# Optimization experiments

Measured on AMD Instinct MI355X. Metric: run time of the kernel, lower is better.

The kernel has to match this reference:

```python
import jax, jax.numpy as jnp
import numpy as np

H = 4      # heads
D = 32     # per-head / input channel dim
B, N = 1, 256


def setup_inputs() -> dict:
    key = jax.random.key(0)
    ks = jax.random.split(key, 10)
    x = jax.random.normal(ks[0], (B, N, N, D), dtype=jnp.float32)
    # binary key mask (1 = keep, 0 = masked out)
    mask = (jax.random.uniform(ks[1], (B, N, N)) > 0.15).astype(jnp.float32)
    s = 1.0 / np.sqrt(D)
    Wq = jax.random.normal(ks[2], (H * D, D), dtype=jnp.float32) * s
    bq = jnp.zeros((H * D,), dtype=jnp.float32)
    Wk = jax.random.normal(ks[3], (H * D, D), dtype=jnp.float32) * s
    bk = jnp.zeros((H * D,), dtype=jnp.float32)
    Wv = jax.random.normal(ks[4], (H * D, D), dtype=jnp.float32) * s
    bv = jnp.zeros((H * D,), dtype=jnp.float32)
    Wb = jax.random.normal(ks[5], (H, D), dtype=jnp.float32) * s
    bb = jnp.zeros((H,), dtype=jnp.float32)
    return {"x": x, "mask": mask, "Wq": Wq, "bq": bq, "Wk": Wk, "bk": bk,
            "Wv": Wv, "bv": bv, "Wb": Wb, "bb": bb}


def reference(x, mask, Wq, bq, Wk, bk, Wv, bv, Wb, bb):
    b_, i_, j_, d_ = x.shape
    # QKV projections -> [B, I, J, H, D]
    q = (x @ Wq.T + bq).reshape(b_, i_, j_, H, d_)
    k = (x @ Wk.T + bk).reshape(b_, i_, j_, H, d_)
    v = (x @ Wv.T + bv).reshape(b_, i_, j_, H, d_)
    # pairwise triangle bias: [B, I, J, H] -> [B, H, J, K]
    tri_b = jnp.transpose(x @ Wb.T + bb, (0, 3, 1, 2))
    scale = 1.0 / jnp.sqrt(jnp.asarray(d_, x.dtype))
    # scores over the key index k along the row: [B, H, I, J, K]
    scores = jnp.einsum('bijhd,bikhd->bhijk', q, k) * scale
    scores = scores + tri_b[:, :, None, :, :]                 # triangle bias
    scores = scores + (mask - 1.0)[:, None, :, None, :] * 1e9  # key mask
    attn = jax.nn.softmax(scores, axis=-1)
    out = jnp.einsum('bhijk,bikhd->bijhd', attn, v)  # [B, I, J, H, D]
    return out
```

## Files before the change

kernel.cpp:

```cpp
#include <hip/hip_runtime.h>

#define HEADS 4
#define NN 256
#define DW 32
#define LOG2E 1.4426950408889634f
#define MASKBIG 1.442695e9f

typedef __bf16 bf16x8 __attribute__((ext_vector_type(8)));
typedef float f32x4 __attribute__((ext_vector_type(4)));
typedef float f32x16 __attribute__((ext_vector_type(16)));
typedef unsigned int u32x4 __attribute__((ext_vector_type(4)));
typedef unsigned short ushort4v __attribute__((ext_vector_type(4)));

static __device__ __forceinline__ ushort f2bf(float f) {
  __bf16 h = (__bf16)f;
  ushort r;
  __builtin_memcpy(&r, &h, 2);
  return r;
}

static __device__ __forceinline__ unsigned cvt_pk_bf16(float lo, float hi) {
  unsigned r;
  asm("v_cvt_pk_bf16_f32 %0, %1, %2" : "=v"(r) : "v"(lo), "v"(hi));
  return r;
}

__global__ __launch_bounds__(256) void bias_kernel(
    const float* __restrict__ x, const float* __restrict__ Wb,
    const float* __restrict__ bb, float* __restrict__ bias2) {
  __shared__ float xs[NN * 36];

  const int q = blockIdx.x;
  const int t = threadIdx.x;

  const float* xr = x + q * (NN * DW);
#pragma unroll
  for (int cc = 0; cc < 8; ++cc) {
    const int f = (cc * 256 + t) * 4;
    const float4 v = *reinterpret_cast<const float4*>(xr + f);
    const int k = f >> 5;
    const int d = f & 31;
    *reinterpret_cast<float4*>(&xs[k * 36 + d]) = v;
  }
  __syncthreads();

  float xv[DW];
#pragma unroll
  for (int c = 0; c < 8; ++c) {
    const float4 v = *reinterpret_cast<const float4*>(&xs[t * 36 + c * 4]);
    xv[c * 4 + 0] = v.x; xv[c * 4 + 1] = v.y;
    xv[c * 4 + 2] = v.z; xv[c * 4 + 3] = v.w;
  }

  const int kb = t >> 5;
  const int c2 = t & 31;
  const int e = c2 & 3;
  const int hi = (c2 >> 2) & 1;
  const int g = c2 >> 3;

#pragma unroll
  for (int h = 0; h < HEADS; ++h) {
    float a0 = 0.f, a1 = 0.f;
#pragma unroll
    for (int d = 0; d < DW; d += 2) {
      a0 += xv[d] * Wb[h * DW + d];
      a1 += xv[d + 1] * Wb[h * DW + d + 1];
    }
    bias2[((((h * 8 + kb) * 4 + g) * 2 + hi) * NN + q) * 4 + e] =
        (a0 + a1 + bb[h]) * LOG2E;
  }
}

__global__ __launch_bounds__(256, 3) void attn_mfma(
    const float* __restrict__ x, const float* __restrict__ mask,
    const float* __restrict__ Wq, const float* __restrict__ bq,
    const float* __restrict__ Wk, const float* __restrict__ bk,
    const float* __restrict__ Wv, const float* __restrict__ bv,
    const float* __restrict__ bias2, float* __restrict__ out) {
  __shared__ __align__(16) ushort Kq[NN][40];
  __shared__ __align__(16) ushort Vt[DW][264];
  __shared__ __align__(16) float mk[NN];
  __shared__ __align__(16) float Ls[NN];

  const int i = blockIdx.x;
  const int t = threadIdx.x;
  const int w = t >> 6;
  const int l = t & 63;
  const int lo5 = l & 31;
  const int hi = l >> 5;
  const int lr = l & 15;
  const int lq = l >> 4;
  const int rowbase = w * 64;
  const float scale = 0.17677669529663687f * LOG2E;

  bf16x8 af[4];
#pragma unroll
  for (int rt = 0; rt < 4; ++rt) {
    const float* xr = x + (i * NN + rowbase + rt * 16 + lr) * DW + lq * 8;
#pragma unroll
    for (int jj = 0; jj < 8; ++jj) af[rt][jj] = (__bf16)xr[jj];
  }
  mk[t] = (mask[i * NN + t] - 1.0f) * MASKBIG;

#pragma unroll 1
  for (int h = 0; h < HEADS; ++h) {
    __syncthreads();

    {
      bf16x8 wf[2];
#pragma unroll
      for (int nt = 0; nt < 2; ++nt) {
        const float* rq = Wq + (h * DW + nt * 16 + lr) * DW + lq * 8;
#pragma unroll
        for (int jj = 0; jj < 8; ++jj) wf[nt][jj] = (__bf16)rq[jj];
      }
#pragma unroll
      for (int rt = 0; rt < 4; ++rt) {
#pragma unroll
        for (int nt = 0; nt < 2; ++nt) {
          const int dd = nt * 16 + lr;
          f32x4 z = {0.f, 0.f, 0.f, 0.f};
          f32x4 cq =
              __builtin_amdgcn_mfma_f32_16x16x32_bf16(af[rt], wf[nt], z, 0, 0, 0);
          const float bqv = bq[h * DW + dd];
#pragma unroll
          for (int j = 0; j < 4; ++j)
            Kq[rowbase + rt * 16 + lq * 4 + j][dd] =
                f2bf((cq[j] + bqv) * scale);
        }
      }
    }
    bf16x8 qb[2][2];
#pragma unroll
    for (int qt = 0; qt < 2; ++qt)
#pragma unroll
      for (int dh = 0; dh < 2; ++dh)
        qb[qt][dh] =
            *(const bf16x8*)&Kq[rowbase + qt * 32 + lo5][dh * 16 + 8 * hi];

    {
      bf16x8 wfk[2], wfv[2];
#pragma unroll
      for (int nt = 0; nt < 2; ++nt) {
        const float* rk = Wk + (h * DW + nt * 16 + lr) * DW + lq * 8;
        const float* rv = Wv + (h * DW + nt * 16 + lr) * DW + lq * 8;
#pragma unroll
        for (int jj = 0; jj < 8; ++jj) {
          wfk[nt][jj] = (__bf16)rk[jj];
          wfv[nt][jj] = (__bf16)rv[jj];
        }
      }
#pragma unroll
      for (int rt = 0; rt < 4; ++rt) {
#pragma unroll
        for (int nt = 0; nt < 2; ++nt) {
          const int dd = nt * 16 + lr;
          f32x4 z = {0.f, 0.f, 0.f, 0.f};
          f32x4 ck =
              __builtin_amdgcn_mfma_f32_16x16x32_bf16(af[rt], wfk[nt], z, 0, 0, 0);
          f32x4 cv =
              __builtin_amdgcn_mfma_f32_16x16x32_bf16(af[rt], wfv[nt], z, 0, 0, 0);
          const float bkv = bk[h * DW + dd];
          const float bvv = bv[h * DW + dd];
#pragma unroll
          for (int j = 0; j < 4; ++j)
            Kq[rowbase + rt * 16 + lq * 4 + j][dd] = f2bf(ck[j] + bkv);
          ushort4v v4;
#pragma unroll
          for (int j = 0; j < 4; ++j) v4[j] = f2bf(cv[j] + bvv);
          *(ushort4v*)&Vt[dd][rowbase + rt * 16 + lq * 4] = v4;
        }
      }
    }
    __syncthreads();

    f32x16 ot[2];
    float lsum[2] = {0.f, 0.f};
#pragma unroll
    for (int qt = 0; qt < 2; ++qt)
#pragma unroll
      for (int r = 0; r < 16; ++r) ot[qt][r] = 0.f;

    const float* btl = bias2 + h * (8 * 4 * 2 * NN * 4) + hi * (NN * 4);

    f32x4 bc[4], bn[4];
    {
      const float* p = btl + (rowbase + lo5) * 4;
#pragma unroll
      for (int g = 0; g < 4; ++g) bc[g] = *(const f32x4*)(p + g * (2 * NN * 4));
    }

#pragma unroll 1
    for (int kb = 0; kb < 8; ++kb) {
      const int kbase = kb * 32;
      const bf16x8 ka0 = *(const bf16x8*)&Kq[kbase + lo5][8 * hi];
      const bf16x8 ka1 = *(const bf16x8*)&Kq[kbase + lo5][16 + 8 * hi];
      const bf16x8 va0 = *(const bf16x8*)&Vt[lo5][kbase + 8 * hi];
      const bf16x8 va1 = *(const bf16x8*)&Vt[lo5][kbase + 16 + 8 * hi];
      float4 mt4[4];
#pragma unroll
      for (int g = 0; g < 4; ++g)
        mt4[g] = *(const float4*)&mk[kbase + 4 * hi + 8 * g];

      auto tile = [&](const int qt, const f32x4 bcur[4]) {
        f32x16 cc;
#pragma unroll
        for (int g = 0; g < 4; ++g)
#pragma unroll
          for (int e = 0; e < 4; ++e)
            cc[g * 4 + e] = bcur[g][e] + (&mt4[g].x)[e];
        __builtin_amdgcn_s_setprio(1);
        f32x16 st =
            __builtin_amdgcn_mfma_f32_32x32x16_bf16(ka0, qb[qt][0], cc, 0, 0, 0);
        st = __builtin_amdgcn_mfma_f32_32x32x16_bf16(ka1, qb[qt][1], st, 0, 0, 0);
        __builtin_amdgcn_s_setprio(0);

#pragma unroll
        for (int r = 0; r < 16; ++r) st[r] = __builtin_amdgcn_exp2f(st[r]);
        float s0 = (st[0] + st[1]) + (st[2] + st[3]);
        float s1 = (st[4] + st[5]) + (st[6] + st[7]);
        float s2 = (st[8] + st[9]) + (st[10] + st[11]);
        float s3 = (st[12] + st[13]) + (st[14] + st[15]);
        lsum[qt] += (s0 + s1) + (s2 + s3);

#pragma unroll
        for (int half = 0; half < 2; ++half) {
          const int b0 = half * 8;
          unsigned w0, w1, w2, w3;
          {
            unsigned A = cvt_pk_bf16(st[b0 + 0], st[b0 + 1]);
            unsigned B = cvt_pk_bf16(st[b0 + 4], st[b0 + 5]);
            asm volatile("v_permlane32_swap_b32 %0, %1" : "+v"(A), "+v"(B));
            w0 = A; w2 = B;
          }
          {
            unsigned A = cvt_pk_bf16(st[b0 + 2], st[b0 + 3]);
            unsigned B = cvt_pk_bf16(st[b0 + 6], st[b0 + 7]);
            asm volatile("v_permlane32_swap_b32 %0, %1" : "+v"(A), "+v"(B));
            w1 = A; w3 = B;
          }
          u32x4 words = {w0, w1, w2, w3};
          const bf16x8 pf = __builtin_bit_cast(bf16x8, words);
          __builtin_amdgcn_s_setprio(1);
          ot[qt] = __builtin_amdgcn_mfma_f32_32x32x16_bf16(
              pf, half ? va1 : va0, ot[qt], 0, 0, 0);
          __builtin_amdgcn_s_setprio(0);
        }
      };

      {
        const float* p = btl + kb * (8 * NN * 4) + (rowbase + 32 + lo5) * 4;
#pragma unroll
        for (int g = 0; g < 4; ++g) bn[g] = *(const f32x4*)(p + g * (2 * NN * 4));
        tile(0, bc);
#pragma unroll
        for (int g = 0; g < 4; ++g) bc[g] = bn[g];
      }
      {
        const int kbn = (kb + 1) & 7;
        const float* p = btl + kbn * (8 * NN * 4) + (rowbase + lo5) * 4;
#pragma unroll
        for (int g = 0; g < 4; ++g) bn[g] = *(const f32x4*)(p + g * (2 * NN * 4));
        tile(1, bc);
#pragma unroll
        for (int g = 0; g < 4; ++g) bc[g] = bn[g];
      }
    }

#pragma unroll
    for (int qt = 0; qt < 2; ++qt) {
      const float ls = lsum[qt] + __shfl_xor(lsum[qt], 32);
      Ls[rowbase + qt * 32 + lo5] = 1.0f / ls;
    }

#pragma unroll
    for (int qt = 0; qt < 2; ++qt)
#pragma unroll
      for (int r = 0; r < 16; ++r) {
        const int qp = (r & 3) + 8 * (r >> 2) + 4 * hi;
        const int qrow = rowbase + qt * 32 + qp;
        out[((i * NN + qrow) * HEADS + h) * DW + lo5] = ot[qt][r] * Ls[qrow];
      }
  }
}

extern "C" void kernel_launch(void* const* d_in, const int* in_sizes, int n_in,
                              void* d_out, int out_size, void* d_ws,
                              size_t ws_size, hipStream_t stream) {
  const float* x    = (const float*)d_in[0];
  const float* mask = (const float*)d_in[1];
  const float* Wq   = (const float*)d_in[2];
  const float* bq   = (const float*)d_in[3];
  const float* Wk   = (const float*)d_in[4];
  const float* bk   = (const float*)d_in[5];
  const float* Wv   = (const float*)d_in[6];
  const float* bv   = (const float*)d_in[7];
  const float* Wb   = (const float*)d_in[8];
  const float* bb   = (const float*)d_in[9];
  float* out = (float*)d_out;
  float* bias2 = (float*)d_ws;

  bias_kernel<<<NN, 256, 0, stream>>>(x, Wb, bb, bias2);
  attn_mfma<<<NN, 256, 0, stream>>>(x, mask, Wq, bq, Wk, bk, Wv, bv,
                                    bias2, out);
}
```

Before: 127.6 us.

## Split heads across blocks so each block handles one (row, head) pair

Launches one block per row and head instead of looping over the four heads inside a block, giving 1024 blocks rather than 256. This fills more of the GPU's compute units and drops the per-head barriers. The bias prefetch double-buffering is replaced by direct loads inside a macro tile body. In exchange, each block reloads and converts its x row tile and mask, so x loads quadruple, and the bias loads are no longer prefetched ahead of use.

```diff
diff --git a/kernel.cpp b/kernel.cpp
--- a/kernel.cpp
+++ b/kernel.cpp
@@ -70,6 +70,64 @@
         (a0 + a1 + bb[h]) * LOG2E;
   }
 }
+
+#define TILE_BODY(QT, QB0, QB1, OT, LS)                                       \
+  {                                                                           \
+    const float* p =                                                          \
+        btl + kb * (8 * NN * 4) + (rowbase + (QT)*32 + lo5) * 4;              \
+    const f32x4 b0 = *(const f32x4*)(p);                                      \
+    const f32x4 b1 = *(const f32x4*)(p + 2 * NN * 4);                         \
+    const f32x4 b2 = *(const f32x4*)(p + 4 * NN * 4);                         \
+    const f32x4 b3 = *(const f32x4*)(p + 6 * NN * 4);                         \
+    f32x16 cc;                                                                \
+    cc[0] = b0[0] + mt0[0]; cc[1] = b0[1] + mt0[1];                           \
+    cc[2] = b0[2] + mt0[2]; cc[3] = b0[3] + mt0[3];                           \
+    cc[4] = b1[0] + mt1[0]; cc[5] = b1[1] + mt1[1];                           \
+    cc[6] = b1[2] + mt1[2]; cc[7] = b1[3] + mt1[3];                           \
+    cc[8] = b2[0] + mt2[0]; cc[9] = b2[1] + mt2[1];                           \
+    cc[10] = b2[2] + mt2[2]; cc[11] = b2[3] + mt2[3];                         \
+    cc[12] = b3[0] + mt3[0]; cc[13] = b3[1] + mt3[1];                         \
+    cc[14] = b3[2] + mt3[2]; cc[15] = b3[3] + mt3[3];                         \
+    __builtin_amdgcn_s_setprio(1);                                            \
+    f32x16 st = __builtin_amdgcn_mfma_f32_32x32x16_bf16(ka0, QB0, cc, 0, 0, 0);\
+    st = __builtin_amdgcn_mfma_f32_32x32x16_bf16(ka1, QB1, st, 0, 0, 0);      \
+    __builtin_amdgcn_s_setprio(0);                                            \
+    _Pragma("unroll")                                                         \
+    for (int r = 0; r < 16; ++r) st[r] = __builtin_amdgcn_exp2f(st[r]);       \
+    {                                                                         \
+      float s0 = (st[0] + st[1]) + (st[2] + st[3]);                           \
+      float s1 = (st[4] + st[5]) + (st[6] + st[7]);                           \
+      float s2 = (st[8] + st[9]) + (st[10] + st[11]);                         \
+      float s3 = (st[12] + st[13]) + (st[14] + st[15]);                       \
+      LS += (s0 + s1) + (s2 + s3);                                            \
+    }                                                                         \
+    {                                                                         \
+      unsigned A0 = cvt_pk_bf16(st[0], st[1]);                                \
+      unsigned B0 = cvt_pk_bf16(st[4], st[5]);                                \
+      asm volatile("v_permlane32_swap_b32 %0, %1" : "+v"(A0), "+v"(B0));      \
+      unsigned A1 = cvt_pk_bf16(st[2], st[3]);                                \
+      unsigned B1 = cvt_pk_bf16(st[6], st[7]);                                \
+      asm volatile("v_permlane32_swap_b32 %0, %1" : "+v"(A1), "+v"(B1));      \
+      u32x4 words = {A0, A1, B0, B1};                                         \
+      const bf16x8 pf = __builtin_bit_cast(bf16x8, words);                    \
+      __builtin_amdgcn_s_setprio(1);                                          \
+      OT = __builtin_amdgcn_mfma_f32_32x32x16_bf16(pf, va0, OT, 0, 0, 0);     \
+      __builtin_amdgcn_s_setprio(0);                                          \
+    }                                                                         \
+    {                                                                         \
+      unsigned A0 = cvt_pk_bf16(st[8], st[9]);                                \
+      unsigned B0 = cvt_pk_bf16(st[12], st[13]);                              \
+      asm volatile("v_permlane32_swap_b32 %0, %1" : "+v"(A0), "+v"(B0));      \
+      unsigned A1 = cvt_pk_bf16(st[10], st[11]);                              \
+      unsigned B1 = cvt_pk_bf16(st[14], st[15]);                              \
+      asm volatile("v_permlane32_swap_b32 %0, %1" : "+v"(A1), "+v"(B1));      \
+      u32x4 words = {A0, A1, B0, B1};                                         \
+      const bf16x8 pf = __builtin_bit_cast(bf16x8, words);                    \
+      __builtin_amdgcn_s_setprio(1);                                          \
+      OT = __builtin_amdgcn_mfma_f32_32x32x16_bf16(pf, va1, OT, 0, 0, 0);     \
+      __builtin_amdgcn_s_setprio(0);                                          \
+    }                                                                         \
+  }
 
 __global__ __launch_bounds__(256, 3) void attn_mfma(
     const float* __restrict__ x, const float* __restrict__ mask,
@@ -82,7 +140,9 @@
   __shared__ __align__(16) float mk[NN];
   __shared__ __align__(16) float Ls[NN];
 
-  const int i = blockIdx.x;
+  const int bid = blockIdx.x;
+  const int i = bid >> 2;
+  const int h = bid & 3;
   const int t = threadIdx.x;
   const int w = t >> 6;
   const int l = t & 63;
@@ -100,187 +160,110 @@
 #pragma unroll
     for (int jj = 0; jj < 8; ++jj) af[rt][jj] = (__bf16)xr[jj];
   }
+
+  {
+    bf16x8 wf[2];
+#pragma unroll
+    for (int nt = 0; nt < 2; ++nt) {
+      const float* rq = Wq + (h * DW + nt * 16 + lr) * DW + lq * 8;
+#pragma unroll
+      for (int jj = 0; jj < 8; ++jj) wf[nt][jj] = (__bf16)rq[jj];
+    }
+#pragma unroll
+    for (int rt = 0; rt < 4; ++rt) {
+#pragma unroll
+      for (int nt = 0; nt < 2; ++nt) {
+        const int dd = nt * 16 + lr;
+        f32x4 z = {0.f, 0.f, 0.f, 0.f};
+        f32x4 cq =
+            __builtin_amdgcn_mfma_f32_16x16x32_bf16(af[rt], wf[nt], z, 0, 0, 0);
+        const float bqv = bq[h * DW + dd];
+#pragma unroll
+        for (int j = 0; j < 4; ++j)
+          Kq[rowbase + rt * 16 + lq * 4 + j][dd] = f2bf((cq[j] + bqv) * scale);
+      }
+    }
+  }
+  bf16x8 qb00, qb01, qb10, qb11;
+  qb00 = *(const bf16x8*)&Kq[rowbase + lo5][8 * hi];
+  qb01 = *(const bf16x8*)&Kq[rowbase + lo5][16 + 8 * hi];
+  qb10 = *(const bf16x8*)&Kq[rowbase + 32 + lo5][8 * hi];
+  qb11 = *(const bf16x8*)&Kq[rowbase + 32 + lo5][16 + 8 * hi];
+
+  {
+    bf16x8 wfk[2], wfv[2];
+#pragma unroll
+    for (int nt = 0; nt < 2; ++nt) {
+      const float* rk = Wk + (h * DW + nt * 16 + lr) * DW + lq * 8;
+      const float* rv = Wv + (h * DW + nt * 16 + lr) * DW + lq * 8;
+#pragma unroll
+      for (int jj = 0; jj < 8; ++jj) {
+        wfk[nt][jj] = (__bf16)rk[jj];
+        wfv[nt][jj] = (__bf16)rv[jj];
+      }
+    }
+#pragma unroll
+    for (int rt = 0; rt < 4; ++rt) {
+#pragma unroll
+      for (int nt = 0; nt < 2; ++nt) {
+        const int dd = nt * 16 + lr;
+        f32x4 z = {0.f, 0.f, 0.f, 0.f};
+        f32x4 ck =
+            __builtin_amdgcn_mfma_f32_16x16x32_bf16(af[rt], wfk[nt], z, 0, 0, 0);
+        f32x4 cv =
+            __builtin_amdgcn_mfma_f32_16x16x32_bf16(af[rt], wfv[nt], z, 0, 0, 0);
+        const float bkv = bk[h * DW + dd];
+        const float bvv = bv[h * DW + dd];
+#pragma unroll
+        for (int j = 0; j < 4; ++j)
+          Kq[rowbase + rt * 16 + lq * 4 + j][dd] = f2bf(ck[j] + bkv);
+        ushort4v v4;
+#pragma unroll
+        for (int j = 0; j < 4; ++j) v4[j] = f2bf(cv[j] + bvv);
+        *(ushort4v*)&Vt[dd][rowbase + rt * 16 + lq * 4] = v4;
+      }
+    }
+  }
   mk[t] = (mask[i * NN + t] - 1.0f) * MASKBIG;
+  __syncthreads();
+
+  f32x16 ot0, ot1;
+  float lsum0 = 0.f, lsum1 = 0.f;
+#pragma unroll
+  for (int r = 0; r < 16; ++r) { ot0[r] = 0.f; ot1[r] = 0.f; }
+
+  const float* btl = bias2 + h * (8 * 4 * 2 * NN * 4) + hi * (NN * 4);
 
 #pragma unroll 1
-  for (int h = 0; h < HEADS; ++h) {
-    __syncthreads();
-
-    {
-      bf16x8 wf[2];
-#pragma unroll
-      for (int nt = 0; nt < 2; ++nt) {
-        const float* rq = Wq + (h * DW + nt * 16 + lr) * DW + lq * 8;
-#pragma unroll
-        for (int jj = 0; jj < 8; ++jj) wf[nt][jj] = (__bf16)rq[jj];
-      }
-#pragma unroll
-      for (int rt = 0; rt < 4; ++rt) {
-#pragma unroll
-        for (int nt = 0; nt < 2; ++nt) {
-          const int dd = nt * 16 + lr;
-          f32x4 z = {0.f, 0.f, 0.f, 0.f};
-          f32x4 cq =
-              __builtin_amdgcn_mfma_f32_16x16x32_bf16(af[rt], wf[nt], z, 0, 0, 0);
-          const float bqv = bq[h * DW + dd];
-#pragma unroll
-          for (int j = 0; j < 4; ++j)
-            Kq[rowbase + rt * 16 + lq * 4 + j][dd] =
-                f2bf((cq[j] + bqv) * scale);
-        }
-      }
-    }
-    bf16x8 qb[2][2];
-#pragma unroll
-    for (int qt = 0; qt < 2; ++qt)
-#pragma unroll
-      for (int dh = 0; dh < 2; ++dh)
-        qb[qt][dh] =
-            *(const bf16x8*)&Kq[rowbase + qt * 32 + lo5][dh * 16 + 8 * hi];
-
-    {
-      bf16x8 wfk[2], wfv[2];
-#pragma unroll
-      for (int nt = 0; nt < 2; ++nt) {
-        const float* rk = Wk + (h * DW + nt * 16 + lr) * DW + lq * 8;
-        const float* rv = Wv + (h * DW + nt * 16 + lr) * DW + lq * 8;
-#pragma unroll
-        for (int jj = 0; jj < 8; ++jj) {
-          wfk[nt][jj] = (__bf16)rk[jj];
-          wfv[nt][jj] = (__bf16)rv[jj];
-        }
-      }
-#pragma unroll
-      for (int rt = 0; rt < 4; ++rt) {
-#pragma unroll
-        for (int nt = 0; nt < 2; ++nt) {
-          const int dd = nt * 16 + lr;
-          f32x4 z = {0.f, 0.f, 0.f, 0.f};
-          f32x4 ck =
-              __builtin_amdgcn_mfma_f32_16x16x32_bf16(af[rt], wfk[nt], z, 0, 0, 0);
-          f32x4 cv =
-              __builtin_amdgcn_mfma_f32_16x16x32_bf16(af[rt], wfv[nt], z, 0, 0, 0);
-          const float bkv = bk[h * DW + dd];
-          const float bvv = bv[h * DW + dd];
-#pragma unroll
-          for (int j = 0; j < 4; ++j)
-            Kq[rowbase + rt * 16 + lq * 4 + j][dd] = f2bf(ck[j] + bkv);
-          ushort4v v4;
-#pragma unroll
-          for (int j = 0; j < 4; ++j) v4[j] = f2bf(cv[j] + bvv);
-          *(ushort4v*)&Vt[dd][rowbase + rt * 16 + lq * 4] = v4;
-        }
-      }
-    }
-    __syncthreads();
-
-    f32x16 ot[2];
-    float lsum[2] = {0.f, 0.f};
-#pragma unroll
-    for (int qt = 0; qt < 2; ++qt)
-#pragma unroll
-      for (int r = 0; r < 16; ++r) ot[qt][r] = 0.f;
-
-    const float* btl = bias2 + h * (8 * 4 * 2 * NN * 4) + hi * (NN * 4);
-
-    f32x4 bc[4], bn[4];
-    {
-      const float* p = btl + (rowbase + lo5) * 4;
-#pragma unroll
-      for (int g = 0; g < 4; ++g) bc[g] = *(const f32x4*)(p + g * (2 * NN * 4));
-    }
-
-#pragma unroll 1
-    for (int kb = 0; kb < 8; ++kb) {
-      const int kbase = kb * 32;
-      const bf16x8 ka0 = *(const bf16x8*)&Kq[kbase + lo5][8 * hi];
-      const bf16x8 ka1 = *(const bf16x8*)&Kq[kbase + lo5][16 + 8 * hi];
-      const bf16x8 va0 = *(const bf16x8*)&Vt[lo5][kbase + 8 * hi];
-      const bf16x8 va1 = *(const bf16x8*)&Vt[lo5][kbase + 16 + 8 * hi];
-      float4 mt4[4];
-#pragma unroll
-      for (int g = 0; g < 4; ++g)
-        mt4[g] = *(const float4*)&mk[kbase + 4 * hi + 8 * g];
-
-      auto tile = [&](const int qt, const f32x4 bcur[4]) {
-        f32x16 cc;
-#pragma unroll
-        for (int g = 0; g < 4; ++g)
-#pragma unroll
-          for (int e = 0; e < 4; ++e)
-            cc[g * 4 + e] = bcur[g][e] + (&mt4[g].x)[e];
-        __builtin_amdgcn_s_setprio(1);
-        f32x16 st =
-            __builtin_amdgcn_mfma_f32_32x32x16_bf16(ka0, qb[qt][0], cc, 0, 0, 0);
-        st = __builtin_amdgcn_mfma_f32_32x32x16_bf16(ka1, qb[qt][1], st, 0, 0, 0);
-        __builtin_amdgcn_s_setprio(0);
-
-#pragma unroll
-        for (int r = 0; r < 16; ++r) st[r] = __builtin_amdgcn_exp2f(st[r]);
-        float s0 = (st[0] + st[1]) + (st[2] + st[3]);
-        float s1 = (st[4] + st[5]) + (st[6] + st[7]);
-        float s2 = (st[8] + st[9]) + (st[10] + st[11]);
-        float s3 = (st[12] + st[13]) + (st[14] + st[15]);
-        lsum[qt] += (s0 + s1) + (s2 + s3);
-
-#pragma unroll
-        for (int half = 0; half < 2; ++half) {
-          const int b0 = half * 8;
-          unsigned w0, w1, w2, w3;
-          {
-            unsigned A = cvt_pk_bf16(st[b0 + 0], st[b0 + 1]);
-            unsigned B = cvt_pk_bf16(st[b0 + 4], st[b0 + 5]);
-            asm volatile("v_permlane32_swap_b32 %0, %1" : "+v"(A), "+v"(B));
-            w0 = A; w2 = B;
-          }
-          {
-            unsigned A = cvt_pk_bf16(st[b0 + 2], st[b0 + 3]);
-            unsigned B = cvt_pk_bf16(st[b0 + 6], st[b0 + 7]);
-            asm volatile("v_permlane32_swap_b32 %0, %1" : "+v"(A), "+v"(B));
-            w1 = A; w3 = B;
-          }
-          u32x4 words = {w0, w1, w2, w3};
-          const bf16x8 pf = __builtin_bit_cast(bf16x8, words);
-          __builtin_amdgcn_s_setprio(1);
-          ot[qt] = __builtin_amdgcn_mfma_f32_32x32x16_bf16(
-              pf, half ? va1 : va0, ot[qt], 0, 0, 0);
-          __builtin_amdgcn_s_setprio(0);
-        }
-      };
-
-      {
-        const float* p = btl + kb * (8 * NN * 4) + (rowbase + 32 + lo5) * 4;
-#pragma unroll
-        for (int g = 0; g < 4; ++g) bn[g] = *(const f32x4*)(p + g * (2 * NN * 4));
-        tile(0, bc);
-#pragma unroll
-        for (int g = 0; g < 4; ++g) bc[g] = bn[g];
-      }
-      {
-        const int kbn = (kb + 1) & 7;
-        const float* p = btl + kbn * (8 * NN * 4) + (rowbase + lo5) * 4;
-#pragma unroll
-        for (int g = 0; g < 4; ++g) bn[g] = *(const f32x4*)(p + g * (2 * NN * 4));
-        tile(1, bc);
-#pragma unroll
-        for (int g = 0; g < 4; ++g) bc[g] = bn[g];
-      }
-    }
-
-#pragma unroll
-    for (int qt = 0; qt < 2; ++qt) {
-      const float ls = lsum[qt] + __shfl_xor(lsum[qt], 32);
-      Ls[rowbase + qt * 32 + lo5] = 1.0f / ls;
-    }
-
-#pragma unroll
-    for (int qt = 0; qt < 2; ++qt)
-#pragma unroll
-      for (int r = 0; r < 16; ++r) {
-        const int qp = (r & 3) + 8 * (r >> 2) + 4 * hi;
-        const int qrow = rowbase + qt * 32 + qp;
-        out[((i * NN + qrow) * HEADS + h) * DW + lo5] = ot[qt][r] * Ls[qrow];
-      }
+  for (int kb = 0; kb < 8; ++kb) {
+    const int kbase = kb * 32;
+    const bf16x8 ka0 = *(const bf16x8*)&Kq[kbase + lo5][8 * hi];
+    const bf16x8 ka1 = *(const bf16x8*)&Kq[kbase + lo5][16 + 8 * hi];
+    const bf16x8 va0 = *(const bf16x8*)&Vt[lo5][kbase + 8 * hi];
+    const bf16x8 va1 = *(const bf16x8*)&Vt[lo5][kbase + 16 + 8 * hi];
+    const f32x4 mt0 = *(const f32x4*)&mk[kbase + 4 * hi];
+    const f32x4 mt1 = *(const f32x4*)&mk[kbase + 4 * hi + 8];
+    const f32x4 mt2 = *(const f32x4*)&mk[kbase + 4 * hi + 16];
+    const f32x4 mt3 = *(const f32x4*)&mk[kbase + 4 * hi + 24];
+
+    TILE_BODY(0, qb00, qb01, ot0, lsum0)
+    TILE_BODY(1, qb10, qb11, ot1, lsum1)
+  }
+
+  {
+    const float l0 = lsum0 + __shfl_xor(lsum0, 32);
+    const float l1 = lsum1 + __shfl_xor(lsum1, 32);
+    Ls[rowbase + lo5] = 1.0f / l0;
+    Ls[rowbase + 32 + lo5] = 1.0f / l1;
+  }
+
+#pragma unroll
+  for (int r = 0; r < 16; ++r) {
+    const int qp = (r & 3) + 8 * (r >> 2) + 4 * hi;
+    const int q0 = rowbase + qp;
+    const int q1 = rowbase + 32 + qp;
+    out[((i * NN + q0) * HEADS + h) * DW + lo5] = ot0[r] * Ls[q0];
+    out[((i * NN + q1) * HEADS + h) * DW + lo5] = ot1[r] * Ls[q1];
   }
 }
 
@@ -301,6 +284,6 @@
   float* bias2 = (float*)d_ws;
 
   bias_kernel<<<NN, 256, 0, stream>>>(x, Wb, bb, bias2);
-  attn_mfma<<<NN, 256, 0, stream>>>(x, mask, Wq, bq, Wk, bk, Wv, bv,
-                                    bias2, out);
-}
+  attn_mfma<<<NN * HEADS, 256, 0, stream>>>(x, mask, Wq, bq, Wk, bk, Wv, bv,
+                                            bias2, out);
+}
```

After: 116.4 us. -8.7%, faster.
